# Performance work log

Hardware: AMD Instinct MI355X
Metric: run time of the kernel (lower is better)

The kernel has to match this reference:

```python
import jax, jax.numpy as jnp
import numpy as np

B, T, F, D, H, L, DFF, G = 4, 2048, 512, 1024, 16, 2, 4096, 16
WSCALE = 0.03  # ~1/sqrt(D) so activations stay well-conditioned


def setup_inputs() -> dict:
    key = jax.random.key(0)
    ks = iter(jax.random.split(key, 24))

    def w(shape):
        return jax.random.normal(next(ks), shape, jnp.float32) * WSCALE

    return {
        "x": jax.random.normal(next(ks), (B, T, F), jnp.float32),
        "proj_w": w((D, F)), "proj_b": jnp.zeros((D,), jnp.float32),
        "wq": w((L, D, D)), "wk": w((L, D, D)), "wv": w((L, D, D)),
        "bq": jnp.zeros((L, D), jnp.float32), "bk": jnp.zeros((L, D), jnp.float32), "bv": jnp.zeros((L, D), jnp.float32),
        "wo": w((L, D, D)), "bo": jnp.zeros((L, D), jnp.float32),
        "ln1_g": jnp.ones((L, D), jnp.float32), "ln1_b": jnp.zeros((L, D), jnp.float32),
        "ln2_g": jnp.ones((L, D), jnp.float32), "ln2_b": jnp.zeros((L, D), jnp.float32),
        "w1": w((L, DFF, D)), "b1": jnp.zeros((L, DFF), jnp.float32),
        "w2": w((L, D, DFF)), "b2": jnp.zeros((L, D), jnp.float32),
        "hw1": w((G, D, D)), "hb1": jnp.zeros((G, D), jnp.float32),
        "hw2": w((G, 2, D)), "hb2": jnp.zeros((G, 2), jnp.float32),
        "nhead": H,
    }


def _ln(x, g, b, eps=1e-5):
    m = x.mean(-1, keepdims=True)
    v = ((x - m) ** 2).mean(-1, keepdims=True)
    return (x - m) * jax.lax.rsqrt(v + eps) * g + b


def _pe(t, d):
    # sinusoidal positional encoding, shape (t, d) (d even -> sin/cos interleave)
    pos = jnp.arange(t, dtype=jnp.float32)[:, None]
    div = jnp.exp(jnp.arange(0, d, 2, dtype=jnp.float32) * (-np.log(10000.0) / d))
    ph = pos * div
    return jnp.stack([jnp.sin(ph), jnp.cos(ph)], axis=-1).reshape(t, d)


def reference(x, proj_w, proj_b, wq, wk, wv, bq, bk, bv, wo, bo,
              ln1_g, ln1_b, ln2_g, ln2_b, w1, b1, w2, b2,
              hw1, hb1, hw2, hb2, nhead):
    Bx, Tx, _ = x.shape
    Dm = proj_w.shape[0]
    dh = Dm // nhead
    h = x @ proj_w.T + proj_b + _pe(Tx, Dm)  # (B,T,D)
    for l in range(wq.shape[0]):  # post-norm encoder layers
        q = (h @ wq[l].T + bq[l]).reshape(Bx, Tx, nhead, dh)
        k = (h @ wk[l].T + bk[l]).reshape(Bx, Tx, nhead, dh)
        v = (h @ wv[l].T + bv[l]).reshape(Bx, Tx, nhead, dh)
        # explicit (non-fused) attention path, as forced by need_weights=True
        scores = jnp.einsum('bthd,bshd->bhts', q, k) / jnp.sqrt(jnp.float32(dh))
        attn = jax.nn.softmax(scores, axis=-1)  # (B,H,T,T)
        ctx = jnp.einsum('bhts,bshd->bthd', attn, v).reshape(Bx, Tx, Dm)
        h = _ln(h + ctx @ wo[l].T + bo[l], ln1_g[l], ln1_b[l])
        ff = jax.nn.relu(h @ w1[l].T + b1[l]) @ w2[l].T + b2[l]
        h = _ln(h + ff, ln2_g[l], ln2_b[l])
    hl = h[:, -1, :]  # last-token pooling, (B,D)
    z = jax.nn.relu(jnp.einsum('bd,gkd->bgk', hl, hw1) + hb1)  # per-sector hidden
    logits = jnp.einsum('bgk,gok->bgo', z, hw2) + hb2           # (B,G,2)
    return jax.nn.softmax(logits, axis=-1)
```

## Files before the change

kernel.cpp:

```cpp
#include <hip/hip_runtime.h>
#include <hip/hip_bf16.h>
#include <cstdint>
#include <cstddef>


typedef __bf16 bf16_t;
typedef __attribute__((ext_vector_type(8))) __bf16 bf16x8;
typedef __attribute__((ext_vector_type(4))) __bf16 bf16x4;
typedef __attribute__((ext_vector_type(4))) float f32x4;
typedef __attribute__((ext_vector_type(16))) float f32x16;
typedef __attribute__((ext_vector_type(2))) unsigned u32x2;
typedef __attribute__((ext_vector_type(4))) unsigned u32x4;

#define DEV __device__ __forceinline__
#define AS1 __attribute__((address_space(1)))
#define AS3 __attribute__((address_space(3)))

DEV void gload_lds16(const void* g, void* l) {
  __builtin_amdgcn_global_load_lds((AS1 void*)(g), (AS3 void*)(l), 16, 0, 0);
}

DEV const char* swz_ptr(const void* base, int row, int colb) {
  return (const char*)base + row * 128 + ((((colb >> 4) ^ (row & 7))) << 4) +
         (colb & 15);
}

DEV unsigned cvtpk(float lo, float hi) {
  unsigned r;
  asm("v_cvt_pk_bf16_f32 %0, %1, %2" : "=v"(r) : "v"(lo), "v"(hi));
  return r;
}
DEV void swap32(unsigned& a, unsigned& b) {
  u32x2 r = __builtin_amdgcn_permlane32_swap(a, b, false, false);
  a = r[0];
  b = r[1];
}
DEV bf16x8 mkfrag(unsigned w0, unsigned w1, unsigned w2, unsigned w3) {
  u32x4 v = {w0, w1, w2, w3};
  return __builtin_bit_cast(bf16x8, v);
}

__global__ __launch_bounds__(256) void f2b_kernel(const float* __restrict__ s,
                                                  bf16_t* __restrict__ d, int n4) {
  const int i = blockIdx.x * 256 + threadIdx.x;
  if (i >= n4) return;
  const float4 v = *(const float4*)&s[(size_t)i * 4];
  bf16x4 o = {(bf16_t)v.x, (bf16_t)v.y, (bf16_t)v.z, (bf16_t)v.w};
  *(bf16x4*)&d[(size_t)i * 4] = o;
}

__global__ __launch_bounds__(256) void bcat_kernel(const float* __restrict__ bq,
                                                   const float* __restrict__ bk,
                                                   const float* __restrict__ bv,
                                                   float* __restrict__ out) {
  const int idx = blockIdx.x * 256 + threadIdx.x;
  const int l = idx / 3072, r = idx - l * 3072;
  const int p = r >> 10, i = r & 1023;
  const float* s = (p == 0) ? bq : ((p == 1) ? bk : bv);
  out[idx] = s[l * 1024 + i];
}

__global__ __launch_bounds__(256) void pe_kernel(float* __restrict__ pe) {
  const int idx = blockIdx.x * 256 + threadIdx.x;
  const int t = idx >> 9, i = idx & 511;
  const float dv = __expf((float)(2 * i) * -0.008994473019508785f);
  const float ph = (float)t * dv;
  pe[(size_t)t * 1024 + 2 * i] = sinf(ph);
  pe[(size_t)t * 1024 + 2 * i + 1] = cosf(ph);
}

template <int EPI, int BM, int BN>
__global__ __launch_bounds__(BM == 256 ? 512 : 256, 2) void gemm9(
    const bf16_t* __restrict__ A, const bf16_t* __restrict__ W,
    const float* __restrict__ bias, bf16_t* __restrict__ outb,
    float* __restrict__ outf, const float* __restrict__ res32,
    const float* __restrict__ pe, int M, int N, int K) {
  constexpr int T = (BM == 256) ? 512 : 256;
  constexpr int RPC = T / 8;
  constexpr int NA = (BM * 128) / (T * 16);
  constexpr int NB = (BN * 128) / (T * 16);
  constexpr int LPT = NA + NB;
  constexpr int MF = (BM == 256) ? 8 : 4;
  constexpr int ASZ = BM * 128;
  constexpr int BUFSZ = (BM + BN) * 128;
  __shared__ char smem[2][BUFSZ];
  const int tid = threadIdx.x, wv = tid >> 6, ln = tid & 63;
  const int nwg = gridDim.x * gridDim.y;
  int bid = blockIdx.y * gridDim.x + blockIdx.x;
  bid = (bid & 7) * (nwg >> 3) + (bid >> 3);
  const int m0 = (bid / gridDim.x) * BM, n0 = (bid % gridDim.x) * BN;
  const int wrow = (BM == 256) ? (wv >> 2) * 128 : (wv >> 1) * 64;
  const int wcol = (BM == 256) ? (wv & 3) * 64 : (wv & 1) * 64;
  f32x4 acc[MF][4] = {};

  const int tp = tid ^ ((tid >> 3) & 7);
  const int srow = tp >> 3, sc8 = (tp & 7) * 8;
  const bf16_t* pa[NA];
  const bf16_t* pb[NB];
#pragma unroll
  for (int u = 0; u < NA; ++u) pa[u] = A + (size_t)(m0 + u * RPC + srow) * K + sc8;
#pragma unroll
  for (int u = 0; u < NB; ++u) pb[u] = W + (size_t)(n0 + u * RPC + srow) * K + sc8;
  const int wvb = wv * 1024;

  auto stage = [&](int s) {
    char* bA = &smem[s][0] + wvb;
    char* bB = &smem[s][ASZ] + wvb;
#pragma unroll
    for (int u = 0; u < NA; ++u) {
      gload_lds16(pa[u], bA + u * (T * 16));
      pa[u] += 64;
    }
#pragma unroll
    for (int u = 0; u < NB; ++u) {
      gload_lds16(pb[u], bB + u * (T * 16));
      pb[u] += 64;
    }
  };

  auto wait_lpt = [&]() {
    if constexpr (LPT == 8)
      asm volatile("s_waitcnt vmcnt(8)" ::: "memory");
    else
      asm volatile("s_waitcnt vmcnt(6)" ::: "memory");
  };

  const int NK = K >> 6;
  stage(0);
  stage(1);
  wait_lpt();
  __builtin_amdgcn_s_barrier();

  for (int kt = 0; kt < NK; ++kt) {
    const char* bA = &smem[kt & 1][0];
    const char* bB = &smem[kt & 1][ASZ];
#pragma unroll
    for (int ks = 0; ks < 2; ++ks) {
      const int cb = ks * 64 + (ln >> 4) * 16;
      bf16x8 bF[4];
#pragma unroll
      for (int n = 0; n < 4; ++n) {
        const int lb = (wcol + n * 16 + (ln & 15)) * 128 + cb;
        bF[n] = *(const bf16x8*)(bB + (lb ^ (((lb >> 7) & 7) << 4)));
      }
#pragma unroll
      for (int mh = 0; mh < 2; ++mh) {
        bf16x8 aF[MF / 2];
#pragma unroll
        for (int m = 0; m < MF / 2; ++m) {
          const int lb = (wrow + (mh * (MF / 2) + m) * 16 + (ln & 15)) * 128 + cb;
          aF[m] = *(const bf16x8*)(bA + (lb ^ (((lb >> 7) & 7) << 4)));
        }
        __builtin_amdgcn_s_setprio(1);
#pragma unroll
        for (int m = 0; m < MF / 2; ++m)
#pragma unroll
          for (int n = 0; n < 4; ++n)
            acc[mh * (MF / 2) + m][n] = __builtin_amdgcn_mfma_f32_16x16x32_bf16(
                aF[m], bF[n], acc[mh * (MF / 2) + m][n], 0, 0, 0);
        __builtin_amdgcn_s_setprio(0);
      }
    }
    __builtin_amdgcn_s_barrier();
    if (kt + 2 < NK) {
      stage(kt & 1);
      wait_lpt();
    } else if (kt + 1 < NK) {
      asm volatile("s_waitcnt vmcnt(0)" ::: "memory");
    }
    __builtin_amdgcn_s_barrier();
    __builtin_amdgcn_sched_barrier(0);
  }

  const int rr = (ln >> 4) * 4, cc = ln & 15;
#pragma unroll
  for (int m = 0; m < MF; ++m) {
    const int rowb = m0 + wrow + m * 16 + rr;
#pragma unroll
    for (int n = 0; n < 4; ++n) {
      const int col = n0 + wcol + n * 16 + cc;
      const float bv = bias[col];
#pragma unroll
      for (int r = 0; r < 4; ++r) {
        const int row = rowb + r;
        float v = acc[m][n][r] + bv;
        const size_t o = (size_t)row * N + col;
        if constexpr (EPI == 1) {
          v = fmaxf(v, 0.f);
          outb[o] = (bf16_t)v;
        } else if constexpr (EPI == 2) {
          v += pe[(size_t)(row & 2047) * 1024 + col];
          outb[o] = (bf16_t)v;
          outf[o] = v;
        } else if constexpr (EPI == 3) {
          v += res32[o];
          outf[o] = v;
        } else {
          outb[o] = (bf16_t)v;
        }
      }
    }
  }
}

__global__ __launch_bounds__(256) void ln_kernel(const float* __restrict__ pre,
                                                 const float* __restrict__ g,
                                                 const float* __restrict__ b,
                                                 bf16_t* __restrict__ h16,
                                                 float* __restrict__ h32) {
  const int row = blockIdx.x, tid = threadIdx.x;
  const size_t base = (size_t)row * 1024 + tid * 4;
  const float4 v = *(const float4*)&pre[base];
  float s = v.x + v.y + v.z + v.w;
  float s2 = v.x * v.x + v.y * v.y + v.z * v.z + v.w * v.w;
#pragma unroll
  for (int m = 1; m < 64; m <<= 1) {
    s += __shfl_xor(s, m);
    s2 += __shfl_xor(s2, m);
  }
  __shared__ float ls[4], ls2[4];
  if ((tid & 63) == 0) {
    ls[tid >> 6] = s;
    ls2[tid >> 6] = s2;
  }
  __syncthreads();
  s = ls[0] + ls[1] + ls[2] + ls[3];
  s2 = ls2[0] + ls2[1] + ls2[2] + ls2[3];
  const float mean = s * (1.f / 1024.f);
  const float var = s2 * (1.f / 1024.f) - mean * mean;
  const float rs = rsqrtf(var + 1e-5f);
  const float4 gv = *(const float4*)&g[tid * 4];
  const float4 bv = *(const float4*)&b[tid * 4];
  const float o0 = (v.x - mean) * rs * gv.x + bv.x;
  const float o1 = (v.y - mean) * rs * gv.y + bv.y;
  const float o2 = (v.z - mean) * rs * gv.z + bv.z;
  const float o3 = (v.w - mean) * rs * gv.w + bv.w;
  bf16x4 ob = {(bf16_t)o0, (bf16_t)o1, (bf16_t)o2, (bf16_t)o3};
  *(bf16x4*)&h16[base] = ob;
  float4 of = {o0, o1, o2, o3};
  *(float4*)&h32[base] = of;
}

__global__ __launch_bounds__(256) void transpose_v(const bf16_t* __restrict__ v,
                                                   bf16_t* __restrict__ vt) {
  __shared__ bf16_t tile[64][80];
  const int bh = blockIdx.y, t0 = blockIdx.x * 64;
  const int tid = threadIdx.x;
  const int b = bh >> 4;
  const size_t vbase = ((size_t)(b * 2048 + t0)) * 3072 + (bh & 15) * 64;
#pragma unroll
  for (int p = 0; p < 2; ++p) {
    const int chunk = p * 256 + tid;
    const int tr = chunk >> 3, c8 = (chunk & 7) * 8;
    *(bf16x8*)&tile[tr][c8] = *(const bf16x8*)&v[vbase + (size_t)tr * 3072 + c8];
  }
  __syncthreads();
  const int d = tid >> 2, t8 = (tid & 3) * 16;
  bf16_t tmp[16];
#pragma unroll
  for (int j = 0; j < 16; ++j) tmp[j] = tile[t8 + j][d];
  const size_t obase = ((size_t)bh * 64 + d) * 2048 + t0 + t8;
  *(bf16x8*)&vt[obase] = *(bf16x8*)&tmp[0];
  *(bf16x8*)&vt[obase + 8] = *(bf16x8*)&tmp[8];
}

__global__ __launch_bounds__(256, 3) void attn_kernel(const bf16_t* __restrict__ qkv,
                                                      const bf16_t* __restrict__ vt,
                                                      bf16_t* __restrict__ ctx) {
  constexpr float SCL = 0.18033688011112042f;
  constexpr int QS = 3072;
  __shared__ bf16_t lK[2][64 * 64];
  __shared__ bf16_t lV[2][64 * 64];
  const int tid = threadIdx.x, wv = tid >> 6, ln = tid & 63;
  const int nwg = gridDim.x * gridDim.y;
  int bid = blockIdx.y * gridDim.x + blockIdx.x;
  bid = (bid & 7) * (nwg >> 3) + (bid >> 3);
  const int bh = bid / gridDim.x, b = bh >> 4, h = bh & 15;
  const int q0 = (bid % gridDim.x) * 128 + wv * 32;
  const int lq = ln & 31, hi = ln >> 5;
  const bf16_t* qp = qkv + (size_t)(b * 2048 + q0 + lq) * QS + h * 64 + hi * 8;
  bf16x8 qF[4];
#pragma unroll
  for (int kk = 0; kk < 4; ++kk) qF[kk] = *(const bf16x8*)(qp + kk * 16);
  f32x16 O0 = {}, O1 = {};
  float m_q = -1e30f, l_q = 0.f;
  const int sr = tid >> 3;
  const int scS = ((tid & 7) ^ ((tid >> 3) & 7)) * 8;
  const bf16_t* kp0 = qkv + 1024 + (size_t)(b * 2048 + sr) * QS + h * 64 + scS;
  const bf16_t* kp1 = kp0 + (size_t)32 * QS;
  const bf16_t* vp0 = vt + (size_t)bh * 64 * 2048 + (size_t)sr * 2048 + scS;
  const bf16_t* vp1 = vp0 + 32 * 2048;

  auto stage = [&](int bufi) {
    char* dk = (char*)&lK[bufi][0] + wv * 1024;
    char* dv = (char*)&lV[bufi][0] + wv * 1024;
    gload_lds16(kp0, dk);
    gload_lds16(kp1, dk + 4096);
    gload_lds16(vp0, dv);
    gload_lds16(vp1, dv + 4096);
    kp0 += (size_t)64 * QS;
    kp1 += (size_t)64 * QS;
    vp0 += 64;
    vp1 += 64;
  };

  stage(0);
  asm volatile("s_waitcnt vmcnt(0)" ::: "memory");
  __builtin_amdgcn_s_barrier();

  for (int st = 0; st < 32; ++st) {
    const int cur = st & 1;
    if (st + 1 < 32) stage(cur ^ 1);
    f32x16 s0 = {}, s1 = {};
    __builtin_amdgcn_s_setprio(1);
#pragma unroll
    for (int kk = 0; kk < 4; ++kk) {
      const int cb = kk * 32 + hi * 16;
      const bf16x8 k0 = *(const bf16x8*)swz_ptr(&lK[cur][0], lq, cb);
      const bf16x8 k1 = *(const bf16x8*)swz_ptr(&lK[cur][0], 32 + lq, cb);
      s0 = __builtin_amdgcn_mfma_f32_32x32x16_bf16(k0, qF[kk], s0, 0, 0, 0);
      s1 = __builtin_amdgcn_mfma_f32_32x32x16_bf16(k1, qF[kk], s1, 0, 0, 0);
    }
    __builtin_amdgcn_s_setprio(0);
    float t[8];
#pragma unroll
    for (int i = 0; i < 8; ++i)
      t[i] = fmaxf(fmaxf(s0[2 * i], s0[2 * i + 1]),
                   fmaxf(s1[2 * i], s1[2 * i + 1]));
    const float u0 = fmaxf(fmaxf(t[0], t[1]), fmaxf(t[2], t[3]));
    const float u1 = fmaxf(fmaxf(t[4], t[5]), fmaxf(t[6], t[7]));
    float mx = fmaxf(u0, u1) * SCL;
    mx = fmaxf(mx, __shfl_xor(mx, 32));
    if (__any(mx > m_q + 8.f)) {
      const float mnew = fmaxf(m_q, mx);
      const float alpha = exp2f(m_q - mnew);
      m_q = mnew;
      l_q *= alpha;
#pragma unroll
      for (int r = 0; r < 16; ++r) {
        const float ar = __shfl(alpha, (r & 3) + 8 * (r >> 2) + 4 * hi);
        O0[r] *= ar;
        O1[r] *= ar;
      }
    }
    float ra = 0.f, rb = 0.f, rc = 0.f, rd = 0.f;
#pragma unroll
    for (int i = 0; i < 4; ++i) {
      s0[i] = exp2f(fmaf(s0[i], SCL, -m_q));
      ra += s0[i];
      s0[i + 4] = exp2f(fmaf(s0[i + 4], SCL, -m_q));
      rb += s0[i + 4];
      s0[i + 8] = exp2f(fmaf(s0[i + 8], SCL, -m_q));
      rc += s0[i + 8];
      s0[i + 12] = exp2f(fmaf(s0[i + 12], SCL, -m_q));
      rd += s0[i + 12];
    }
#pragma unroll
    for (int i = 0; i < 4; ++i) {
      s1[i] = exp2f(fmaf(s1[i], SCL, -m_q));
      ra += s1[i];
      s1[i + 4] = exp2f(fmaf(s1[i + 4], SCL, -m_q));
      rb += s1[i + 4];
      s1[i + 8] = exp2f(fmaf(s1[i + 8], SCL, -m_q));
      rc += s1[i + 8];
      s1[i + 12] = exp2f(fmaf(s1[i + 12], SCL, -m_q));
      rd += s1[i + 12];
    }
    float rsum = (ra + rb) + (rc + rd);
    rsum += __shfl_xor(rsum, 32);
    l_q += rsum;
    __builtin_amdgcn_s_setprio(1);
    {
      unsigned A = cvtpk(s0[0], s0[1]), Bq = cvtpk(s0[2], s0[3]);
      unsigned C = cvtpk(s0[4], s0[5]), Dq = cvtpk(s0[6], s0[7]);
      unsigned A2 = cvtpk(s0[8], s0[9]), B2 = cvtpk(s0[10], s0[11]);
      unsigned C2 = cvtpk(s0[12], s0[13]), D2 = cvtpk(s0[14], s0[15]);
      swap32(A, C);
      swap32(Bq, Dq);
      swap32(A2, C2);
      swap32(B2, D2);
      const bf16x8 f0 = mkfrag(A, Bq, C, Dq);
      const bf16x8 f1 = mkfrag(A2, B2, C2, D2);
      const bf16x8 v00 = *(const bf16x8*)swz_ptr(&lV[cur][0], lq, 0 + hi * 16);
      const bf16x8 v01 = *(const bf16x8*)swz_ptr(&lV[cur][0], lq, 32 + hi * 16);
      const bf16x8 v10 = *(const bf16x8*)swz_ptr(&lV[cur][0], 32 + lq, 0 + hi * 16);
      const bf16x8 v11 = *(const bf16x8*)swz_ptr(&lV[cur][0], 32 + lq, 32 + hi * 16);
      O0 = __builtin_amdgcn_mfma_f32_32x32x16_bf16(f0, v00, O0, 0, 0, 0);
      O0 = __builtin_amdgcn_mfma_f32_32x32x16_bf16(f1, v01, O0, 0, 0, 0);
      O1 = __builtin_amdgcn_mfma_f32_32x32x16_bf16(f0, v10, O1, 0, 0, 0);
      O1 = __builtin_amdgcn_mfma_f32_32x32x16_bf16(f1, v11, O1, 0, 0, 0);
    }
    {
      unsigned A = cvtpk(s1[0], s1[1]), Bq = cvtpk(s1[2], s1[3]);
      unsigned C = cvtpk(s1[4], s1[5]), Dq = cvtpk(s1[6], s1[7]);
      unsigned A2 = cvtpk(s1[8], s1[9]), B2 = cvtpk(s1[10], s1[11]);
      unsigned C2 = cvtpk(s1[12], s1[13]), D2 = cvtpk(s1[14], s1[15]);
      swap32(A, C);
      swap32(Bq, Dq);
      swap32(A2, C2);
      swap32(B2, D2);
      const bf16x8 f2 = mkfrag(A, Bq, C, Dq);
      const bf16x8 f3 = mkfrag(A2, B2, C2, D2);
      const bf16x8 v02 = *(const bf16x8*)swz_ptr(&lV[cur][0], lq, 64 + hi * 16);
      const bf16x8 v03 = *(const bf16x8*)swz_ptr(&lV[cur][0], lq, 96 + hi * 16);
      const bf16x8 v12 = *(const bf16x8*)swz_ptr(&lV[cur][0], 32 + lq, 64 + hi * 16);
      const bf16x8 v13 = *(const bf16x8*)swz_ptr(&lV[cur][0], 32 + lq, 96 + hi * 16);
      O0 = __builtin_amdgcn_mfma_f32_32x32x16_bf16(f2, v02, O0, 0, 0, 0);
      O0 = __builtin_amdgcn_mfma_f32_32x32x16_bf16(f3, v03, O0, 0, 0, 0);
      O1 = __builtin_amdgcn_mfma_f32_32x32x16_bf16(f2, v12, O1, 0, 0, 0);
      O1 = __builtin_amdgcn_mfma_f32_32x32x16_bf16(f3, v13, O1, 0, 0, 0);
    }
    __builtin_amdgcn_s_setprio(0);
    asm volatile("s_waitcnt vmcnt(0)" ::: "memory");
    __builtin_amdgcn_s_barrier();
    __builtin_amdgcn_sched_barrier(0);
  }
  const float invl = 1.f / l_q;
  const size_t obase = ((size_t)(b * 2048 + q0)) * 1024 + h * 64 + lq;
#pragma unroll
  for (int r = 0; r < 16; ++r) {
    const int qr = (r & 3) + 8 * (r >> 2) + 4 * hi;
    const float iv = __shfl(invl, qr);
    ctx[obase + (size_t)qr * 1024] = (bf16_t)(O0[r] * iv);
    ctx[obase + (size_t)qr * 1024 + 32] = (bf16_t)(O1[r] * iv);
  }
}

__global__ __launch_bounds__(256) void head_z(const float* __restrict__ h32,
                                              const float* __restrict__ hw1,
                                              const float* __restrict__ hb1,
                                              float* __restrict__ z) {
  const int g = blockIdx.x, slab = blockIdx.y;
  const int wv = threadIdx.x >> 6, ln = threadIdx.x & 63;
  float4 hl[4][4];
#pragma unroll
  for (int b = 0; b < 4; ++b)
#pragma unroll
    for (int c = 0; c < 4; ++c)
      hl[b][c] = *(const float4*)&h32[((size_t)b * 2048 + 2047) * 1024 + c * 256 + ln * 4];
  const int k0 = slab * 64 + wv * 16;
  for (int kk = 0; kk < 16; ++kk) {
    const int kq = k0 + kk;
    const float* wrow = hw1 + ((size_t)g * 1024 + kq) * 1024;
    float p[4] = {0, 0, 0, 0};
#pragma unroll
    for (int c = 0; c < 4; ++c) {
      const float4 w4 = *(const float4*)&wrow[c * 256 + ln * 4];
#pragma unroll
      for (int b = 0; b < 4; ++b)
        p[b] += w4.x * hl[b][c].x + w4.y * hl[b][c].y + w4.z * hl[b][c].z +
                w4.w * hl[b][c].w;
    }
#pragma unroll
    for (int m = 1; m < 64; m <<= 1)
#pragma unroll
      for (int b = 0; b < 4; ++b) p[b] += __shfl_xor(p[b], m);
    if (ln == 0) {
#pragma unroll
      for (int b = 0; b < 4; ++b)
        z[((size_t)b * 16 + g) * 1024 + kq] = fmaxf(p[b] + hb1[g * 1024 + kq], 0.f);
    }
  }
}

__global__ __launch_bounds__(64) void head_logits(const float* __restrict__ z,
                                                  const float* __restrict__ hw2,
                                                  const float* __restrict__ hb2,
                                                  float* __restrict__ out) {
  const int b = blockIdx.x, g = blockIdx.y, ln = threadIdx.x;
  const float* zr = z + ((size_t)b * 16 + g) * 1024;
  const float* w0 = hw2 + (size_t)g * 2048;
  const float* w1 = w0 + 1024;
  float p0 = 0.f, p1 = 0.f;
#pragma unroll
  for (int c = 0; c < 4; ++c) {
    const float4 zv = *(const float4*)&zr[c * 256 + ln * 4];
    const float4 a0 = *(const float4*)&w0[c * 256 + ln * 4];
    const float4 a1 = *(const float4*)&w1[c * 256 + ln * 4];
    p0 += zv.x * a0.x + zv.y * a0.y + zv.z * a0.z + zv.w * a0.w;
    p1 += zv.x * a1.x + zv.y * a1.y + zv.z * a1.z + zv.w * a1.w;
  }
#pragma unroll
  for (int m = 1; m < 64; m <<= 1) {
    p0 += __shfl_xor(p0, m);
    p1 += __shfl_xor(p1, m);
  }
  if (ln == 0) {
    const float l0 = p0 + hb2[g * 2], l1 = p1 + hb2[g * 2 + 1];
    const float mx = fmaxf(l0, l1);
    const float e0 = expf(l0 - mx), e1 = expf(l1 - mx);
    const float inv = 1.f / (e0 + e1);
    out[(size_t)b * 32 + g * 2] = e0 * inv;
    out[(size_t)b * 32 + g * 2 + 1] = e1 * inv;
  }
}

extern "C" void kernel_launch(void* const* d_in, const int* in_sizes, int n_in,
                              void* d_out, int out_size, void* d_ws, size_t ws_size,
                              hipStream_t stream) {
  const float* x = (const float*)d_in[0];
  const float* proj_w = (const float*)d_in[1];
  const float* proj_b = (const float*)d_in[2];
  const float* wq = (const float*)d_in[3];
  const float* wk = (const float*)d_in[4];
  const float* wvv = (const float*)d_in[5];
  const float* bq = (const float*)d_in[6];
  const float* bk = (const float*)d_in[7];
  const float* bv = (const float*)d_in[8];
  const float* wo = (const float*)d_in[9];
  const float* bo = (const float*)d_in[10];
  const float* ln1_g = (const float*)d_in[11];
  const float* ln1_b = (const float*)d_in[12];
  const float* ln2_g = (const float*)d_in[13];
  const float* ln2_b = (const float*)d_in[14];
  const float* w1 = (const float*)d_in[15];
  const float* b1 = (const float*)d_in[16];
  const float* w2 = (const float*)d_in[17];
  const float* b2 = (const float*)d_in[18];
  const float* hw1 = (const float*)d_in[19];
  const float* hb1 = (const float*)d_in[20];
  const float* hw2 = (const float*)d_in[21];
  const float* hb2 = (const float*)d_in[22];
  float* out = (float*)d_out;
  char* ws = (char*)d_ws;

  size_t o = 0;
  auto take = [&](size_t bytes) { size_t r = o; o += bytes; return r; };
  const size_t o_wqkv = take(12582912);
  const size_t o_wo = take(4194304);
  const size_t o_w1 = take(16777216);
  const size_t o_w2 = take(16777216);
  const size_t o_pw = take(1048576);
  const size_t o_h16 = take(16777216);
  const size_t o_h32 = take(33554432);
  const size_t o_pre = take(33554432);
  const size_t o_r4 = take(67108864);
  const size_t o_r5 = take(16777216);
  const size_t o_z = take(262144);
  const size_t o_bqkv = take(24576);

  bf16_t* wqkv16 = (bf16_t*)(ws + o_wqkv);
  bf16_t* wo16 = (bf16_t*)(ws + o_wo);
  bf16_t* w1_16 = (bf16_t*)(ws + o_w1);
  bf16_t* w2_16 = (bf16_t*)(ws + o_w2);
  bf16_t* pw16 = (bf16_t*)(ws + o_pw);
  bf16_t* h16 = (bf16_t*)(ws + o_h16);
  float* h32 = (float*)(ws + o_h32);
  float* pre32 = (float*)(ws + o_pre);
  bf16_t* qkv16 = (bf16_t*)(ws + o_r4);
  bf16_t* vT16 = (bf16_t*)(ws + o_r4 + 50331648);
  bf16_t* ff1 = (bf16_t*)(ws + o_r4);
  bf16_t* x16 = (bf16_t*)(ws + o_r5);
  float* pe32 = (float*)(ws + o_r5 + 8388608);
  bf16_t* ctx16 = (bf16_t*)(ws + o_r5);
  float* zbuf = (float*)(ws + o_z);
  float* bqkv = (float*)(ws + o_bqkv);

  f2b_kernel<<<4096, 256, 0, stream>>>(x, x16, 1048576);
  f2b_kernel<<<512, 256, 0, stream>>>(proj_w, pw16, 131072);
  for (int l = 0; l < 2; ++l) {
    f2b_kernel<<<1024, 256, 0, stream>>>(wq + (size_t)l * 1048576,
                                         wqkv16 + (size_t)(l * 3 + 0) * 1048576, 262144);
    f2b_kernel<<<1024, 256, 0, stream>>>(wk + (size_t)l * 1048576,
                                         wqkv16 + (size_t)(l * 3 + 1) * 1048576, 262144);
    f2b_kernel<<<1024, 256, 0, stream>>>(wvv + (size_t)l * 1048576,
                                         wqkv16 + (size_t)(l * 3 + 2) * 1048576, 262144);
  }
  f2b_kernel<<<2048, 256, 0, stream>>>(wo, wo16, 524288);
  f2b_kernel<<<8192, 256, 0, stream>>>(w1, w1_16, 2097152);
  f2b_kernel<<<8192, 256, 0, stream>>>(w2, w2_16, 2097152);
  bcat_kernel<<<24, 256, 0, stream>>>(bq, bk, bv, bqkv);
  pe_kernel<<<4096, 256, 0, stream>>>(pe32);

  gemm9<2, 128, 128><<<dim3(8, 64), 256, 0, stream>>>(x16, pw16, proj_b, h16, h32,
                                                      nullptr, pe32, 8192, 1024, 512);

  for (int l = 0; l < 2; ++l) {
    const bf16_t* wqkv_l = wqkv16 + (size_t)l * 3145728;
    const bf16_t* wo_l = wo16 + (size_t)l * 1048576;
    const bf16_t* w1_l = w1_16 + (size_t)l * 4194304;
    const bf16_t* w2_l = w2_16 + (size_t)l * 4194304;

    gemm9<0, 256, 256><<<dim3(12, 32), 512, 0, stream>>>(h16, wqkv_l, bqkv + l * 3072,
                                                         qkv16, nullptr, nullptr,
                                                         nullptr, 8192, 3072, 1024);
    transpose_v<<<dim3(32, 64), 256, 0, stream>>>(qkv16 + 2048, vT16);
    attn_kernel<<<dim3(16, 64), 256, 0, stream>>>(qkv16, vT16, ctx16);
    gemm9<3, 128, 128><<<dim3(8, 64), 256, 0, stream>>>(ctx16, wo_l, bo + l * 1024,
                                                        nullptr, pre32, h32, nullptr,
                                                        8192, 1024, 1024);
    ln_kernel<<<8192, 256, 0, stream>>>(pre32, ln1_g + l * 1024, ln1_b + l * 1024, h16,
                                        h32);
    gemm9<1, 256, 256><<<dim3(16, 32), 512, 0, stream>>>(h16, w1_l, b1 + l * 4096, ff1,
                                                         nullptr, nullptr, nullptr,
                                                         8192, 4096, 1024);
    gemm9<3, 128, 128><<<dim3(8, 64), 256, 0, stream>>>(ff1, w2_l, b2 + l * 1024,
                                                        nullptr, pre32, h32, nullptr,
                                                        8192, 1024, 4096);
    ln_kernel<<<8192, 256, 0, stream>>>(pre32, ln2_g + l * 1024, ln2_b + l * 1024, h16,
                                        h32);
  }

  head_z<<<dim3(16, 16), 256, 0, stream>>>(h32, hw1, hb1, zbuf);
  head_logits<<<dim3(4, 16), 64, 0, stream>>>(zbuf, hw2, hb2, out);
}
```

Measured before the change: 884.7 us.

## Split attention key block into two halves and retile QKV GEMM to 256x128

The attention inner loop now handles the 64-key tile as two 32-key sub-blocks. Each sub-block runs its own max, rescale, exp and PV MFMA steps, so only one 16-wide score accumulator is live at a time, and the launch bound is raised from 3 to 4 blocks per CU to use the freed registers for occupancy. This adds a second max check and possible rescale per tile and shortens each MFMA burst. Separately, the QKV projection GEMM moves from 256x256 to 256x128 tiles with twice as many workgroups. A WIDE flag keeps the 8-fragment warp layout only for 256x256 tiles.

```diff
diff --git a/kernel.cpp b/kernel.cpp
--- a/kernel.cpp
+++ b/kernel.cpp
@@ -80,7 +80,8 @@
   constexpr int NA = (BM * 128) / (T * 16);
   constexpr int NB = (BN * 128) / (T * 16);
   constexpr int LPT = NA + NB;
-  constexpr int MF = (BM == 256) ? 8 : 4;
+  constexpr bool WIDE = (BM == 256 && BN == 256);
+  constexpr int MF = WIDE ? 8 : 4;
   constexpr int ASZ = BM * 128;
   constexpr int BUFSZ = (BM + BN) * 128;
   __shared__ char smem[2][BUFSZ];
@@ -89,8 +90,8 @@
   int bid = blockIdx.y * gridDim.x + blockIdx.x;
   bid = (bid & 7) * (nwg >> 3) + (bid >> 3);
   const int m0 = (bid / gridDim.x) * BM, n0 = (bid % gridDim.x) * BN;
-  const int wrow = (BM == 256) ? (wv >> 2) * 128 : (wv >> 1) * 64;
-  const int wcol = (BM == 256) ? (wv & 3) * 64 : (wv & 1) * 64;
+  const int wrow = WIDE ? (wv >> 2) * 128 : (wv >> 1) * 64;
+  const int wcol = WIDE ? (wv & 3) * 64 : (wv & 1) * 64;
   f32x4 acc[MF][4] = {};
 
   const int tp = tid ^ ((tid >> 3) & 7);
@@ -264,7 +265,7 @@
   *(bf16x8*)&vt[obase + 8] = *(bf16x8*)&tmp[8];
 }
 
-__global__ __launch_bounds__(256, 3) void attn_kernel(const bf16_t* __restrict__ qkv,
+__global__ __launch_bounds__(256, 4) void attn_kernel(const bf16_t* __restrict__ qkv,
                                                       const bf16_t* __restrict__ vt,
                                                       bf16_t* __restrict__ ctx) {
   constexpr float SCL = 0.18033688011112042f;
@@ -311,106 +312,70 @@
   for (int st = 0; st < 32; ++st) {
     const int cur = st & 1;
     if (st + 1 < 32) stage(cur ^ 1);
-    f32x16 s0 = {}, s1 = {};
-    __builtin_amdgcn_s_setprio(1);
-#pragma unroll
-    for (int kk = 0; kk < 4; ++kk) {
-      const int cb = kk * 32 + hi * 16;
-      const bf16x8 k0 = *(const bf16x8*)swz_ptr(&lK[cur][0], lq, cb);
-      const bf16x8 k1 = *(const bf16x8*)swz_ptr(&lK[cur][0], 32 + lq, cb);
-      s0 = __builtin_amdgcn_mfma_f32_32x32x16_bf16(k0, qF[kk], s0, 0, 0, 0);
-      s1 = __builtin_amdgcn_mfma_f32_32x32x16_bf16(k1, qF[kk], s1, 0, 0, 0);
-    }
-    __builtin_amdgcn_s_setprio(0);
-    float t[8];
-#pragma unroll
-    for (int i = 0; i < 8; ++i)
-      t[i] = fmaxf(fmaxf(s0[2 * i], s0[2 * i + 1]),
-                   fmaxf(s1[2 * i], s1[2 * i + 1]));
-    const float u0 = fmaxf(fmaxf(t[0], t[1]), fmaxf(t[2], t[3]));
-    const float u1 = fmaxf(fmaxf(t[4], t[5]), fmaxf(t[6], t[7]));
-    float mx = fmaxf(u0, u1) * SCL;
-    mx = fmaxf(mx, __shfl_xor(mx, 32));
-    if (__any(mx > m_q + 8.f)) {
-      const float mnew = fmaxf(m_q, mx);
-      const float alpha = exp2f(m_q - mnew);
-      m_q = mnew;
-      l_q *= alpha;
-#pragma unroll
-      for (int r = 0; r < 16; ++r) {
-        const float ar = __shfl(alpha, (r & 3) + 8 * (r >> 2) + 4 * hi);
-        O0[r] *= ar;
-        O1[r] *= ar;
+#pragma unroll
+    for (int sb = 0; sb < 2; ++sb) {
+      f32x16 s = {};
+      __builtin_amdgcn_s_setprio(1);
+#pragma unroll
+      for (int kk = 0; kk < 4; ++kk) {
+        const bf16x8 kf =
+            *(const bf16x8*)swz_ptr(&lK[cur][0], sb * 32 + lq, kk * 32 + hi * 16);
+        s = __builtin_amdgcn_mfma_f32_32x32x16_bf16(kf, qF[kk], s, 0, 0, 0);
       }
-    }
-    float ra = 0.f, rb = 0.f, rc = 0.f, rd = 0.f;
-#pragma unroll
-    for (int i = 0; i < 4; ++i) {
-      s0[i] = exp2f(fmaf(s0[i], SCL, -m_q));
-      ra += s0[i];
-      s0[i + 4] = exp2f(fmaf(s0[i + 4], SCL, -m_q));
-      rb += s0[i + 4];
-      s0[i + 8] = exp2f(fmaf(s0[i + 8], SCL, -m_q));
-      rc += s0[i + 8];
-      s0[i + 12] = exp2f(fmaf(s0[i + 12], SCL, -m_q));
-      rd += s0[i + 12];
-    }
-#pragma unroll
-    for (int i = 0; i < 4; ++i) {
-      s1[i] = exp2f(fmaf(s1[i], SCL, -m_q));
-      ra += s1[i];
-      s1[i + 4] = exp2f(fmaf(s1[i + 4], SCL, -m_q));
-      rb += s1[i + 4];
-      s1[i + 8] = exp2f(fmaf(s1[i + 8], SCL, -m_q));
-      rc += s1[i + 8];
-      s1[i + 12] = exp2f(fmaf(s1[i + 12], SCL, -m_q));
-      rd += s1[i + 12];
-    }
-    float rsum = (ra + rb) + (rc + rd);
-    rsum += __shfl_xor(rsum, 32);
-    l_q += rsum;
-    __builtin_amdgcn_s_setprio(1);
-    {
-      unsigned A = cvtpk(s0[0], s0[1]), Bq = cvtpk(s0[2], s0[3]);
-      unsigned C = cvtpk(s0[4], s0[5]), Dq = cvtpk(s0[6], s0[7]);
-      unsigned A2 = cvtpk(s0[8], s0[9]), B2 = cvtpk(s0[10], s0[11]);
-      unsigned C2 = cvtpk(s0[12], s0[13]), D2 = cvtpk(s0[14], s0[15]);
+      __builtin_amdgcn_s_setprio(0);
+      float t0 = fmaxf(fmaxf(s[0], s[1]), fmaxf(s[2], s[3]));
+      float t1 = fmaxf(fmaxf(s[4], s[5]), fmaxf(s[6], s[7]));
+      float t2 = fmaxf(fmaxf(s[8], s[9]), fmaxf(s[10], s[11]));
+      float t3 = fmaxf(fmaxf(s[12], s[13]), fmaxf(s[14], s[15]));
+      float mx = fmaxf(fmaxf(t0, t1), fmaxf(t2, t3)) * SCL;
+      mx = fmaxf(mx, __shfl_xor(mx, 32));
+      if (__any(mx > m_q + 8.f)) {
+        const float mnew = fmaxf(m_q, mx);
+        const float alpha = exp2f(m_q - mnew);
+        m_q = mnew;
+        l_q *= alpha;
+#pragma unroll
+        for (int r = 0; r < 16; ++r) {
+          const float ar = __shfl(alpha, (r & 3) + 8 * (r >> 2) + 4 * hi);
+          O0[r] *= ar;
+          O1[r] *= ar;
+        }
+      }
+      float ra = 0.f, rb = 0.f;
+#pragma unroll
+      for (int i = 0; i < 8; ++i) {
+        s[i] = exp2f(fmaf(s[i], SCL, -m_q));
+        ra += s[i];
+        s[i + 8] = exp2f(fmaf(s[i + 8], SCL, -m_q));
+        rb += s[i + 8];
+      }
+      float rsum = ra + rb;
+      rsum += __shfl_xor(rsum, 32);
+      l_q += rsum;
+      unsigned A = cvtpk(s[0], s[1]), Bq = cvtpk(s[2], s[3]);
+      unsigned C = cvtpk(s[4], s[5]), Dq = cvtpk(s[6], s[7]);
+      unsigned A2 = cvtpk(s[8], s[9]), B2 = cvtpk(s[10], s[11]);
+      unsigned C2 = cvtpk(s[12], s[13]), D2 = cvtpk(s[14], s[15]);
       swap32(A, C);
       swap32(Bq, Dq);
       swap32(A2, C2);
       swap32(B2, D2);
       const bf16x8 f0 = mkfrag(A, Bq, C, Dq);
       const bf16x8 f1 = mkfrag(A2, B2, C2, D2);
-      const bf16x8 v00 = *(const bf16x8*)swz_ptr(&lV[cur][0], lq, 0 + hi * 16);
-      const bf16x8 v01 = *(const bf16x8*)swz_ptr(&lV[cur][0], lq, 32 + hi * 16);
-      const bf16x8 v10 = *(const bf16x8*)swz_ptr(&lV[cur][0], 32 + lq, 0 + hi * 16);
-      const bf16x8 v11 = *(const bf16x8*)swz_ptr(&lV[cur][0], 32 + lq, 32 + hi * 16);
-      O0 = __builtin_amdgcn_mfma_f32_32x32x16_bf16(f0, v00, O0, 0, 0, 0);
-      O0 = __builtin_amdgcn_mfma_f32_32x32x16_bf16(f1, v01, O0, 0, 0, 0);
-      O1 = __builtin_amdgcn_mfma_f32_32x32x16_bf16(f0, v10, O1, 0, 0, 0);
-      O1 = __builtin_amdgcn_mfma_f32_32x32x16_bf16(f1, v11, O1, 0, 0, 0);
-    }
-    {
-      unsigned A = cvtpk(s1[0], s1[1]), Bq = cvtpk(s1[2], s1[3]);
-      unsigned C = cvtpk(s1[4], s1[5]), Dq = cvtpk(s1[6], s1[7]);
-      unsigned A2 = cvtpk(s1[8], s1[9]), B2 = cvtpk(s1[10], s1[11]);
-      unsigned C2 = cvtpk(s1[12], s1[13]), D2 = cvtpk(s1[14], s1[15]);
-      swap32(A, C);
-      swap32(Bq, Dq);
-      swap32(A2, C2);
-      swap32(B2, D2);
-      const bf16x8 f2 = mkfrag(A, Bq, C, Dq);
-      const bf16x8 f3 = mkfrag(A2, B2, C2, D2);
-      const bf16x8 v02 = *(const bf16x8*)swz_ptr(&lV[cur][0], lq, 64 + hi * 16);
-      const bf16x8 v03 = *(const bf16x8*)swz_ptr(&lV[cur][0], lq, 96 + hi * 16);
-      const bf16x8 v12 = *(const bf16x8*)swz_ptr(&lV[cur][0], 32 + lq, 64 + hi * 16);
-      const bf16x8 v13 = *(const bf16x8*)swz_ptr(&lV[cur][0], 32 + lq, 96 + hi * 16);
-      O0 = __builtin_amdgcn_mfma_f32_32x32x16_bf16(f2, v02, O0, 0, 0, 0);
-      O0 = __builtin_amdgcn_mfma_f32_32x32x16_bf16(f3, v03, O0, 0, 0, 0);
-      O1 = __builtin_amdgcn_mfma_f32_32x32x16_bf16(f2, v12, O1, 0, 0, 0);
-      O1 = __builtin_amdgcn_mfma_f32_32x32x16_bf16(f3, v13, O1, 0, 0, 0);
-    }
-    __builtin_amdgcn_s_setprio(0);
+      __builtin_amdgcn_s_setprio(1);
+      const bf16x8 va = *(const bf16x8*)swz_ptr(&lV[cur][0], lq, sb * 64 + hi * 16);
+      const bf16x8 vb =
+          *(const bf16x8*)swz_ptr(&lV[cur][0], lq, sb * 64 + 32 + hi * 16);
+      const bf16x8 vc =
+          *(const bf16x8*)swz_ptr(&lV[cur][0], 32 + lq, sb * 64 + hi * 16);
+      const bf16x8 vd =
+          *(const bf16x8*)swz_ptr(&lV[cur][0], 32 + lq, sb * 64 + 32 + hi * 16);
+      O0 = __builtin_amdgcn_mfma_f32_32x32x16_bf16(f0, va, O0, 0, 0, 0);
+      O0 = __builtin_amdgcn_mfma_f32_32x32x16_bf16(f1, vb, O0, 0, 0, 0);
+      O1 = __builtin_amdgcn_mfma_f32_32x32x16_bf16(f0, vc, O1, 0, 0, 0);
+      O1 = __builtin_amdgcn_mfma_f32_32x32x16_bf16(f1, vd, O1, 0, 0, 0);
+      __builtin_amdgcn_s_setprio(0);
+    }
     asm volatile("s_waitcnt vmcnt(0)" ::: "memory");
     __builtin_amdgcn_s_barrier();
     __builtin_amdgcn_sched_barrier(0);
@@ -581,7 +546,7 @@
     const bf16_t* w1_l = w1_16 + (size_t)l * 4194304;
     const bf16_t* w2_l = w2_16 + (size_t)l * 4194304;
 
-    gemm9<0, 256, 256><<<dim3(12, 32), 512, 0, stream>>>(h16, wqkv_l, bqkv + l * 3072,
+    gemm9<0, 256, 128><<<dim3(24, 32), 512, 0, stream>>>(h16, wqkv_l, bqkv + l * 3072,
                                                          qkv16, nullptr, nullptr,
                                                          nullptr, 8192, 3072, 1024);
     transpose_v<<<dim3(32, 64), 256, 0, stream>>>(qkv16 + 2048, vT16);
```

Measured after the change: 884.3 us. No clear change (-0.0%).
